# Optimization experiments

Measured on AMD Instinct MI355X. Metric: run time of the kernel, lower is better.

## Reference

```python
import jax, jax.numpy as jnp
import numpy as np

HQ, HKV, DK, DV = 8, 4, 128, 128
WIDTH, CLIP, MAXPOS = 16, 5.0, 2048
EPS = 1e-5

def rms_bn(x, g, ch_axis):
    # EMA_RMSBatchNorm (eval with batch stats): per-channel RMS over all other dims
    axes = tuple(i for i in range(x.ndim) if i != ch_axis)
    ms = jnp.mean(jnp.square(x), axis=axes, keepdims=True)
    shape = [1] * x.ndim; shape[ch_axis] = g.shape[0]
    return x * jax.lax.rsqrt(ms + EPS) * g.reshape(shape)

def ln(x, g, b):
    m = jnp.mean(x, -1, keepdims=True)
    v = jnp.mean(jnp.square(x - m), -1, keepdims=True)
    return (x - m) * jax.lax.rsqrt(v + EPS) * g + b

def rope(x):
    # x: [B,S,H,C], custom AlphaGenome frequency schedule
    B, S, H, C = x.shape
    nf = C // 2
    pos = jnp.arange(S, dtype=x.dtype)
    lin = jnp.arange(nf, dtype=x.dtype)
    end = max(MAXPOS - nf + 1.0, 1.0)
    geom = jnp.exp(jnp.linspace(0.0, np.log(end), nf).astype(x.dtype))
    inv_freq = 1.0 / (lin + geom)
    theta = jnp.repeat(pos[:, None] * inv_freq, 2, axis=-1)[None, :, None, :]  # [1,S,1,C]
    x_rot = jnp.stack([-x[..., 1::2], x[..., ::2]], axis=-1).reshape(x.shape)
    return x * jnp.cos(theta) + x_rot * jnp.sin(theta)

def _forward(x, pair_x, ab_bn_g, ab_fc_w, bn1_g, wq, wk, wv, qn_g, qn_b, kn_g, kn_b,
             vn_g, vn_b, wo, bo, bn2_g, mbn1_g, w1, b1, w2, b2, mbn2_g):
    B, S, C = x.shape
    # --- AttentionBias from pair representation ---
    pb = rms_bn(pair_x, ab_bn_g, 3)
    pb = jax.nn.gelu(pb, approximate=False)
    pb = jnp.einsum('bijc,gc->bijg', pb, ab_fc_w)          # [B,Sp,Sp,group]
    pb = jnp.repeat(jnp.repeat(pb, WIDTH, axis=1), WIDTH, axis=2)  # upsample to [B,S,S,group]
    bias = jnp.repeat(jnp.transpose(pb, (0, 3, 1, 2)), HKV, axis=1)  # [B,HQ,S,S]
    # --- GQA attention ---
    xn = rms_bn(x, bn1_g, 2)
    q = ln((xn @ wq.T).reshape(B, S, HQ, DK), qn_g, qn_b)
    k = ln((xn @ wk.T).reshape(B, S, HKV, DK), kn_g, kn_b)
    v = ln((xn @ wv.T).reshape(B, S, HKV, DV), vn_g, vn_b)
    q = rope(q); k = rope(k)
    rep = HQ // HKV
    k = jnp.tile(k, (1, 1, rep, 1))  # torch .repeat: [k0..k3, k0..k3]
    v = jnp.tile(v, (1, 1, rep, 1))
    logits = jnp.einsum('bshd,bThd->bhsT', q, k) / np.float32(np.sqrt(DK)) + bias
    logits = jnp.tanh(logits / CLIP) * CLIP
    attn = jax.nn.softmax(logits, axis=-1)
    y = jnp.einsum('bhsT,bThd->bshd', attn, v)
    # faithful to original: permute then reshape (layout scramble preserved)
    y = jnp.transpose(y, (0, 2, 1, 3)).reshape(B, S, HQ * DV)
    x = x + rms_bn(y @ wo.T + bo, bn2_g, 2)
    # --- MLP block ---
    h = jax.nn.relu(rms_bn(x, mbn1_g, 2) @ w1.T + b1)
    x = x + rms_bn(h @ w2.T + b2, mbn2_g, 2)
    return x, pair_x

def setup_inputs() -> dict:
    key = jax.random.key(0)
    ks = jax.random.split(key, 10)
    B, S, C, SP, PC = 2, 2048, 768, 128, 128
    n = lambda k, sh: jax.random.normal(k, sh, jnp.float32) * 0.02
    d = {}
    d['x'] = jax.random.normal(ks[0], (B, S, C), jnp.float32)
    d['pair_x'] = jax.random.normal(ks[1], (B, SP, SP, PC), jnp.float32)
    d['ab_bn_g'] = jnp.ones((PC,), jnp.float32)
    d['ab_fc_w'] = n(ks[2], (HQ // HKV, PC))
    d['bn1_g'] = jnp.ones((C,), jnp.float32)
    d['wq'] = n(ks[3], (HQ * DK, C))
    d['wk'] = n(ks[4], (HKV * DK, C))
    d['wv'] = n(ks[5], (HKV * DV, C))
    d['qn_g'] = jnp.ones((DK,), jnp.float32); d['qn_b'] = jnp.zeros((DK,), jnp.float32)
    d['kn_g'] = jnp.ones((DK,), jnp.float32); d['kn_b'] = jnp.zeros((DK,), jnp.float32)
    d['vn_g'] = jnp.ones((DV,), jnp.float32); d['vn_b'] = jnp.zeros((DV,), jnp.float32)
    d['wo'] = n(ks[6], (C, HQ * DV)); d['bo'] = jnp.zeros((C,), jnp.float32)
    d['bn2_g'] = jnp.ones((C,), jnp.float32)
    d['mbn1_g'] = jnp.ones((C,), jnp.float32)
    d['w1'] = n(ks[7], (2 * C, C)); d['b1'] = jnp.zeros((2 * C,), jnp.float32)
    d['w2'] = n(ks[8], (C, 2 * C)); d['b2'] = jnp.zeros((C,), jnp.float32)
    d['mbn2_g'] = jnp.ones((C,), jnp.float32)
    return d

def reference(x, pair_x, ab_bn_g, ab_fc_w, bn1_g, wq, wk, wv, qn_g, qn_b, kn_g, kn_b,
              vn_g, vn_b, wo, bo, bn2_g, mbn1_g, w1, b1, w2, b2, mbn2_g):
    return _forward(x, pair_x, ab_bn_g, ab_fc_w, bn1_g, wq, wk, wv, qn_g, qn_b, kn_g,
                    kn_b, vn_g, vn_b, wo, bo, bn2_g, mbn1_g, w1, b1, w2, b2, mbn2_g)
```

## Files before the change

kernel.cpp:

```cpp
#include <hip/hip_runtime.h>
#include <math.h>

#define EPS 1e-5f

typedef __attribute__((ext_vector_type(8))) short short8;
typedef __attribute__((ext_vector_type(4))) float f32x4;

namespace {

constexpr int Bn = 2, Sn = 2048, Cn = 768;
constexpr float INV_BS = 1.0f / 4096.0f;
constexpr float INV_PAIR = 1.0f / 32768.0f;
constexpr float LOG2E = 1.4426950408889634f;

__device__ __forceinline__ ushort f2bf(float f) {
  uint u = __float_as_uint(f);
  u = (u + 0x7fffu + ((u >> 16) & 1u)) >> 16;
  return (ushort)u;
}
__device__ __forceinline__ float bf2f(ushort u) {
  return __uint_as_float(((uint)u) << 16);
}
__device__ __forceinline__ uint cvt_pk_bf16(float lo, float hi) {
  uint r;
  asm("v_cvt_pk_bf16_f32 %0, %1, %2" : "=v"(r) : "v"(lo), "v"(hi));
  return r;
}
__device__ __forceinline__ void gl16(const ushort* g, ushort* l) {
  __builtin_amdgcn_global_load_lds(
      (const __attribute__((address_space(1))) unsigned int*)(unsigned long long)(size_t)g,
      (__attribute__((address_space(3))) unsigned int*)(unsigned int)(size_t)l, 16, 0, 0);
}

#define KSW(r, c) ((((r) * 128) + (c)) ^ (((r) & 7) * 8))
#define VTW(d, t) ((((d) * 64) + (t)) ^ (((d) & 7) * 8))
#define PSW2(w, q, c) ((w) * 2048 + ((((q) * 64) + (c)) ^ (((q) & 7) * 8)))

__global__ void castall_k(const float* __restrict__ wq, const float* __restrict__ wk,
                          const float* __restrict__ wv, const float* __restrict__ wo,
                          const float* __restrict__ w1, const float* __restrict__ w2,
                          ushort* __restrict__ dst) {
  int u = blockIdx.x * 256 + threadIdx.x;
  const float* src; int local;
  if (u < 98304)       { src = wq; local = u; }
  else if (u < 147456) { src = wk; local = u - 98304; }
  else if (u < 196608) { src = wv; local = u - 147456; }
  else if (u < 294912) { src = wo; local = u - 196608; }
  else if (u < 442368) { src = w1; local = u - 294912; }
  else                 { src = w2; local = u - 442368; }
  int i = local * 8;
  float4 a = *(const float4*)&src[i];
  float4 b = *(const float4*)&src[i + 4];
  union { short8 s8; ushort us[8]; } o;
  o.us[0] = f2bf(a.x); o.us[1] = f2bf(a.y); o.us[2] = f2bf(a.z); o.us[3] = f2bf(a.w);
  o.us[4] = f2bf(b.x); o.us[5] = f2bf(b.y); o.us[6] = f2bf(b.z); o.us[7] = f2bf(b.w);
  *(short8*)&dst[u * 8] = o.s8;
}

__global__ void rope_tab_k(float2* __restrict__ tab) {
  int idx = blockIdx.x * 256 + threadIdx.x;
  int s = idx >> 6, i = idx & 63;
  const float kGeo = logf(1985.0f) * (1.0f / 63.0f);
  float inv = 1.0f / ((float)i + expf((float)i * kGeo));
  float th = (float)s * inv;
  tab[idx] = make_float2(cosf(th), sinf(th));
}

__global__ void scale_cast_k(const float* __restrict__ a, const float* __restrict__ sums,
                             const float* __restrict__ g, ushort* __restrict__ o) {
  int idx = blockIdx.x * 256 + threadIdx.x;
  int c0 = (idx % 96) * 8;
  int base = idx * 8;
  float4 v0 = *(const float4*)&a[base];
  float4 v1 = *(const float4*)&a[base + 4];
  union { short8 s8; ushort us[8]; } r;
  float vv[8] = {v0.x, v0.y, v0.z, v0.w, v1.x, v1.y, v1.z, v1.w};
#pragma unroll
  for (int j = 0; j < 8; ++j) {
    float sc = rsqrtf(sums[c0 + j] * INV_BS + EPS) * g[c0 + j];
    r.us[j] = f2bf(vv[j] * sc);
  }
  *(short8*)&o[base] = r.s8;
}

__global__ void pair_sumsq_k(const float* __restrict__ p, float* __restrict__ out) {
  int r0 = blockIdx.x * 128;
  float acc = 0.f;
  for (int r = 0; r < 128; ++r) {
    float v = p[(size_t)(r0 + r) * 128 + threadIdx.x];
    acc += v * v;
  }
  atomicAdd(&out[threadIdx.x], acc);
}

__global__ void ch_sumsq768_k(const float* __restrict__ a, float* __restrict__ out) {
  int r0 = blockIdx.x * 16;
  int c = threadIdx.x;
  float acc = 0.f;
  for (int r = 0; r < 16; ++r) {
    float v = a[(size_t)(r0 + r) * 768 + c];
    acc += v * v;
  }
  atomicAdd(&out[c], acc);
}

__global__ void pair_bias_k(const float* __restrict__ p, const float* __restrict__ ps,
                            const float* __restrict__ g, const float* __restrict__ w,
                            float* __restrict__ pb2) {
  int idx = blockIdx.x * 128 + threadIdx.x;
  const float* row = p + (size_t)idx * 128;
  float a0 = 0.f, a1 = 0.f;
  for (int c = 0; c < 128; ++c) {
    float sc = rsqrtf(ps[c] * INV_PAIR + EPS) * g[c];
    float v = row[c] * sc;
    float ge = 0.5f * v * (1.f + erff(v * 0.70710678118654752f));
    a0 += ge * w[c];
    a1 += ge * w[128 + c];
  }
  pb2[(size_t)idx * 2 + 0] = a0 * (0.4f * LOG2E);
  pb2[(size_t)idx * 2 + 1] = a1 * (0.4f * LOG2E);
}

template <bool RELU, bool OUT_BF16>
__global__ __launch_bounds__(256) void gemm_bf16_k(
    const ushort* __restrict__ A, const ushort* __restrict__ B,
    void* __restrict__ Cv, int M, int N, int K,
    const float* __restrict__ bias) {
  __shared__ __align__(16) ushort As[128 * 64];
  __shared__ __align__(16) ushort Bs[128 * 64];
  const int m0 = blockIdx.y * 128, n0 = blockIdx.x * 128;
  const int tid = threadIdx.x;
  const int lane = tid & 63;
  const int wid = tid >> 6;
  const int l15 = lane & 15, l4 = lane >> 4;
  const int wm = (wid >> 1) * 64, wn = (wid & 1) * 64;
  const ushort* asrc[4]; const ushort* bsrc[4];
  ushort* adst[4]; ushort* bdst[4];
#pragma unroll
  for (int u = 0; u < 4; ++u) {
    int ci = u * 256 + tid;
    int r = ci >> 3, s = ci & 7, g = s ^ (r & 7);
    asrc[u] = A + (size_t)(m0 + r) * K + g * 8;
    bsrc[u] = B + (size_t)(n0 + r) * K + g * 8;
    adst[u] = &As[(u * 256 + wid * 64) * 8];
    bdst[u] = &Bs[(u * 256 + wid * 64) * 8];
  }
  f32x4 acc[4][4];
#pragma unroll
  for (int i = 0; i < 4; ++i)
#pragma unroll
    for (int j = 0; j < 4; ++j) acc[i][j] = (f32x4){0.f, 0.f, 0.f, 0.f};
  for (int k0 = 0; k0 < K; k0 += 64) {
#pragma unroll
    for (int u = 0; u < 4; ++u) {
      gl16(asrc[u] + k0, adst[u]);
      gl16(bsrc[u] + k0, bdst[u]);
    }
    __syncthreads();
#pragma unroll
    for (int ks = 0; ks < 2; ++ks) {
      const int sw = ((ks * 4 + l4) ^ (l15 & 7)) * 8;
      short8 af[4], bf[4];
#pragma unroll
      for (int i = 0; i < 4; ++i) af[i] = *(const short8*)&As[(wm + i * 16 + l15) * 64 + sw];
#pragma unroll
      for (int j = 0; j < 4; ++j) bf[j] = *(const short8*)&Bs[(wn + j * 16 + l15) * 64 + sw];
#pragma unroll
      for (int i = 0; i < 4; ++i)
#pragma unroll
        for (int j = 0; j < 4; ++j)
          acc[i][j] = __builtin_amdgcn_mfma_f32_16x16x32_bf16(af[i], bf[j], acc[i][j], 0, 0, 0);
    }
    __syncthreads();
  }
  float* Cf = (float*)Cv;
  ushort* Cb = (ushort*)Cv;
#pragma unroll
  for (int j = 0; j < 4; ++j) {
    int col = n0 + wn + j * 16 + l15;
    float bv = bias ? bias[col] : 0.f;
#pragma unroll
    for (int i = 0; i < 4; ++i) {
      int row = m0 + wm + i * 16 + l4 * 4;
#pragma unroll
      for (int r = 0; r < 4; ++r) {
        float v = acc[i][j][r] + bv;
        if (RELU) v = fmaxf(v, 0.f);
        if (OUT_BF16) Cb[(size_t)(row + r) * N + col] = f2bf(v);
        else Cf[(size_t)(row + r) * N + col] = v;
      }
    }
  }
}

template <bool SUMSQ>
__global__ __launch_bounds__(256) void gemm64_bf16_k(
    const ushort* __restrict__ A, const ushort* __restrict__ B,
    float* __restrict__ Cf, int M, int N, int K,
    const float* __restrict__ bias, float* __restrict__ ssq) {
  __shared__ __align__(16) ushort As[64 * 64];
  __shared__ __align__(16) ushort Bs[128 * 64];
  const int m0 = blockIdx.y * 64, n0 = blockIdx.x * 128;
  const int tid = threadIdx.x;
  const int lane = tid & 63;
  const int wid = tid >> 6;
  const int l15 = lane & 15, l4 = lane >> 4;
  const int wn = wid * 32;
  const ushort* asrc[2]; ushort* adst[2];
  const ushort* bsrc[4]; ushort* bdst[4];
#pragma unroll
  for (int u = 0; u < 2; ++u) {
    int ci = u * 256 + tid;
    int r = ci >> 3, s = ci & 7, g = s ^ (r & 7);
    asrc[u] = A + (size_t)(m0 + r) * K + g * 8;
    adst[u] = &As[(u * 256 + wid * 64) * 8];
  }
#pragma unroll
  for (int u = 0; u < 4; ++u) {
    int ci = u * 256 + tid;
    int r = ci >> 3, s = ci & 7, g = s ^ (r & 7);
    bsrc[u] = B + (size_t)(n0 + r) * K + g * 8;
    bdst[u] = &Bs[(u * 256 + wid * 64) * 8];
  }
  f32x4 acc[4][2];
#pragma unroll
  for (int i = 0; i < 4; ++i)
#pragma unroll
    for (int j = 0; j < 2; ++j) acc[i][j] = (f32x4){0.f, 0.f, 0.f, 0.f};
  for (int k0 = 0; k0 < K; k0 += 64) {
#pragma unroll
    for (int u = 0; u < 2; ++u) gl16(asrc[u] + k0, adst[u]);
#pragma unroll
    for (int u = 0; u < 4; ++u) gl16(bsrc[u] + k0, bdst[u]);
    __syncthreads();
#pragma unroll
    for (int ks = 0; ks < 2; ++ks) {
      const int sw = ((ks * 4 + l4) ^ (l15 & 7)) * 8;
      short8 af[4], bf[2];
#pragma unroll
      for (int i = 0; i < 4; ++i) af[i] = *(const short8*)&As[(i * 16 + l15) * 64 + sw];
#pragma unroll
      for (int j = 0; j < 2; ++j) bf[j] = *(const short8*)&Bs[(wn + j * 16 + l15) * 64 + sw];
#pragma unroll
      for (int i = 0; i < 4; ++i)
#pragma unroll
        for (int j = 0; j < 2; ++j)
          acc[i][j] = __builtin_amdgcn_mfma_f32_16x16x32_bf16(af[i], bf[j], acc[i][j], 0, 0, 0);
    }
    __syncthreads();
  }
#pragma unroll
  for (int j = 0; j < 2; ++j) {
    int col = n0 + wn + j * 16 + l15;
    float bv = bias ? bias[col] : 0.f;
    float sq = 0.f;
#pragma unroll
    for (int i = 0; i < 4; ++i) {
      int row = m0 + i * 16 + l4 * 4;
#pragma unroll
      for (int r = 0; r < 4; ++r) {
        float v = acc[i][j][r] + bv;
        if (SUMSQ) sq += v * v;
        Cf[(size_t)(row + r) * N + col] = v;
      }
    }
    if (SUMSQ) {
      sq += __shfl_xor(sq, 16);
      sq += __shfl_xor(sq, 32);
      if (l4 == 0) atomicAdd(&ssq[col], sq);
    }
  }
}

__global__ __launch_bounds__(256) void ln_rope_k(
    const float* __restrict__ qkv, const float2* __restrict__ rtab,
    const float* __restrict__ qg, const float* __restrict__ qb,
    const float* __restrict__ kg, const float* __restrict__ kb,
    const float* __restrict__ vg, const float* __restrict__ vb,
    ushort* __restrict__ q_b, ushort* __restrict__ k_b, ushort* __restrict__ v_b) {
  const int half = threadIdx.x >> 7;
  const int tid = threadIdx.x & 127;
  const int bs = blockIdx.x * 2 + half;
  const int slot = blockIdx.y;
  const int s = bs & (Sn - 1);
  const int b = bs >> 11;
  const float* src; const float* g; const float* be; ushort* dst; bool dorope; bool isq = false;
  if (slot < 8) {
    src = qkv + (size_t)bs * 2048 + slot * 128;
    g = qg; be = qb;
    dst = q_b + ((size_t)(b * 8 + slot) * Sn + s) * 128;
    dorope = true; isq = true;
  } else if (slot < 12) {
    int h = slot - 8;
    src = qkv + (size_t)bs * 2048 + 1024 + h * 128;
    g = kg; be = kb;
    dst = k_b + ((size_t)(b * 4 + h) * Sn + s) * 128;
    dorope = true;
  } else {
    int h = slot - 12;
    src = qkv + (size_t)bs * 2048 + 1536 + h * 128;
    g = vg; be = vb;
    dst = v_b + ((size_t)(b * 4 + h) * Sn + s) * 128;
    dorope = false;
  }
  __shared__ float sh[2][128];
  __shared__ float red[2][4];
  float v = src[tid];
  float sum = v;
#pragma unroll
  for (int o = 32; o >= 1; o >>= 1) sum += __shfl_xor(sum, o);
  if ((tid & 63) == 0) red[half][tid >> 6] = sum;
  __syncthreads();
  float mean = (red[half][0] + red[half][1]) * (1.f / 128.f);
  float d = v - mean;
  float s2 = d * d;
#pragma unroll
  for (int o = 32; o >= 1; o >>= 1) s2 += __shfl_xor(s2, o);
  if ((tid & 63) == 0) red[half][2 + (tid >> 6)] = s2;
  __syncthreads();
  float var = (red[half][2] + red[half][3]) * (1.f / 128.f);
  float val = d * rsqrtf(var + EPS) * g[tid] + be[tid];
  if (dorope) {
    sh[half][tid] = val;
    __syncthreads();
    float2 cssn = rtab[(s << 6) | (tid >> 1)];
    float rot = (tid & 1) ? sh[half][tid - 1] : -sh[half][tid + 1];
    val = val * cssn.x + rot * cssn.y;
  }
  if (isq) val *= 0.035355339059327376f * LOG2E;
  dst[tid] = f2bf(val);
}

__global__ __launch_bounds__(256) void vtrans_k(const ushort* __restrict__ vb,
                                                ushort* __restrict__ vtt) {
  __shared__ __align__(16) ushort T[64][136];
  const int hv = blockIdx.y, s0 = blockIdx.x * 64;
  const int tid = threadIdx.x;
  const ushort* src = vb + ((size_t)hv * Sn + s0) * 128;
#pragma unroll
  for (int u = 0; u < 4; ++u) {
    int fi = u * 256 + tid;
    int r = fi >> 4, c = (fi & 15) * 8;
    *(float4*)&T[r][c] = *(const float4*)&src[(size_t)r * 128 + c];
  }
  __syncthreads();
  ushort* dst = vtt + (size_t)hv * 128 * Sn + s0;
#pragma unroll
  for (int u = 0; u < 4; ++u) {
    int fi = u * 256 + tid;
    int d = fi >> 3, t8 = (fi & 7) * 8;
    union { float4 f4; ushort us[8]; } o;
#pragma unroll
    for (int j = 0; j < 8; ++j) o.us[j] = T[t8 + j][d];
    *(float4*)&dst[(size_t)d * Sn + t8] = o.f4;
  }
}

__global__ __launch_bounds__(256, 2) void flash_v10_k(
    const ushort* __restrict__ qb, const ushort* __restrict__ kb,
    const ushort* __restrict__ vtt, const float* __restrict__ pb2,
    ushort* __restrict__ part_y, float* __restrict__ part_l) {
  __shared__ __align__(16) ushort Ks[64 * 128];
  __shared__ __align__(16) ushort Vt[128 * 64];
  __shared__ __align__(16) ushort Ps[4 * 32 * 64];
  const int s0 = blockIdx.x * 128;
  const int bh = blockIdx.y;
  const int half = blockIdx.z;
  const int b = bh >> 3, h = bh & 7;
  const int kv = h & 3, grp = h >> 2;
  const int tid = threadIdx.x;
  const int wid = tid >> 6, lane = tid & 63;
  const int l15 = lane & 15, l4 = lane >> 4;
  const ushort* kbase = kb + (size_t)(b * 4 + kv) * Sn * 128;
  const ushort* vbase = vtt + (size_t)(b * 4 + kv) * 128 * Sn;
  const int qr0 = s0 + wid * 32;
  short8 qf[2][4];
#pragma unroll
  for (int rg = 0; rg < 2; ++rg)
#pragma unroll
    for (int kc = 0; kc < 4; ++kc)
      qf[rg][kc] = *(const short8*)&qb[((size_t)bh * Sn + qr0 + rg * 16 + l15) * 128 + kc * 32 + l4 * 8];
  const ushort* ksrc[4]; const ushort* vsrc[4];
  ushort* kdst[4]; ushort* vdst[4];
#pragma unroll
  for (int u = 0; u < 4; ++u) {
    int ci = u * 256 + tid;
    int kr = ci >> 4, kg = (ci & 15) ^ (kr & 7);
    ksrc[u] = kbase + (size_t)kr * 128 + kg * 8;
    kdst[u] = &Ks[(u * 256 + wid * 64) * 8];
    int vd = ci >> 3, vg = (ci & 7) ^ (vd & 7);
    vsrc[u] = vbase + (size_t)vd * Sn + vg * 8;
    vdst[u] = &Vt[(u * 256 + wid * 64) * 8];
  }
  f32x4 y[2][8];
#pragma unroll
  for (int rg = 0; rg < 2; ++rg)
#pragma unroll
    for (int i = 0; i < 8; ++i) y[rg][i] = (f32x4){0.f, 0.f, 0.f, 0.f};
  float lsum[2] = {0.f, 0.f};
  const float C2 = -10.f * LOG2E;
  const int tbeg = half * 704;
  const int tend = (half == 2) ? 2048 : tbeg + 704;
  for (int t0 = tbeg; t0 < tend; t0 += 64) {
    __syncthreads();
#pragma unroll
    for (int u = 0; u < 4; ++u) {
      gl16(ksrc[u] + (size_t)t0 * 128, kdst[u]);
      gl16(vsrc[u] + t0, vdst[u]);
    }
    __syncthreads();
    f32x4 acc[2][4];
#pragma unroll
    for (int rg = 0; rg < 2; ++rg)
#pragma unroll
      for (int nb = 0; nb < 4; ++nb) acc[rg][nb] = (f32x4){0.f, 0.f, 0.f, 0.f};
    __builtin_amdgcn_s_setprio(1);
#pragma unroll
    for (int kc = 0; kc < 4; ++kc)
#pragma unroll
      for (int nb = 0; nb < 4; ++nb) {
        short8 kf = *(const short8*)&Ks[KSW(nb * 16 + l15, kc * 32 + l4 * 8)];
        acc[0][nb] = __builtin_amdgcn_mfma_f32_16x16x32_bf16(kf, qf[0][kc], acc[0][nb], 0, 0, 0);
        acc[1][nb] = __builtin_amdgcn_mfma_f32_16x16x32_bf16(kf, qf[1][kc], acc[1][nb], 0, 0, 0);
      }
    __builtin_amdgcn_s_setprio(0);
#pragma unroll
    for (int rg = 0; rg < 2; ++rg)
#pragma unroll
      for (int nb = 0; nb < 4; ++nb) {
        float bias = pb2[(((size_t)b * 128 + (s0 >> 4) + wid * 2 + rg) * 128 + (t0 >> 4) + nb) * 2 + grp];
        float p[4];
#pragma unroll
        for (int r = 0; r < 4; ++r) {
          float e = exp2f(acc[rg][nb][r] + bias);
          p[r] = exp2f(C2 * __builtin_amdgcn_rcpf(e + 1.f));
        }
        lsum[rg] += (p[0] + p[1]) + (p[2] + p[3]);
        uint2 pk;
        pk.x = cvt_pk_bf16(p[0], p[1]);
        pk.y = cvt_pk_bf16(p[2], p[3]);
        *(uint2*)&Ps[PSW2(wid, rg * 16 + l15, nb * 16 + l4 * 4)] = pk;
      }
    __builtin_amdgcn_s_setprio(1);
#pragma unroll
    for (int ks = 0; ks < 2; ++ks) {
      short8 pa0 = *(const short8*)&Ps[PSW2(wid, l15, ks * 32 + l4 * 8)];
      short8 pa1 = *(const short8*)&Ps[PSW2(wid, 16 + l15, ks * 32 + l4 * 8)];
#pragma unroll
      for (int nbd = 0; nbd < 8; ++nbd) {
        short8 vf = *(const short8*)&Vt[VTW(nbd * 16 + l15, ks * 32 + l4 * 8)];
        y[0][nbd] = __builtin_amdgcn_mfma_f32_16x16x32_bf16(pa0, vf, y[0][nbd], 0, 0, 0);
        y[1][nbd] = __builtin_amdgcn_mfma_f32_16x16x32_bf16(pa1, vf, y[1][nbd], 0, 0, 0);
      }
    }
    __builtin_amdgcn_s_setprio(0);
  }
#pragma unroll
  for (int rg = 0; rg < 2; ++rg) {
    float ls = lsum[rg];
    ls += __shfl_xor(ls, 16);
    ls += __shfl_xor(ls, 32);
    if (l4 == 0) part_l[(size_t)(half * 16 + bh) * Sn + qr0 + rg * 16 + l15] = ls;
    ushort* pybase = part_y + ((size_t)(half * 16 + bh) * Sn + qr0 + rg * 16) * 128;
#pragma unroll
    for (int nbd = 0; nbd < 8; ++nbd)
#pragma unroll
      for (int r = 0; r < 4; ++r)
        pybase[(size_t)(l4 * 4 + r) * 128 + nbd * 16 + l15] = f2bf(y[rg][nbd][r]);
  }
}

__global__ void combine_k(const ushort* __restrict__ part_y, const float* __restrict__ part_l,
                          ushort* __restrict__ attn_b) {
  int t = blockIdx.x * 256 + threadIdx.x;
  int row = t >> 4;
  size_t o0 = (size_t)row * 128 + (t & 15) * 8;
  float acc[8] = {};
#pragma unroll
  for (int hf = 0; hf < 3; ++hf) {
    union { short8 s8; ushort us[8]; } u;
    u.s8 = *(const short8*)&part_y[o0 + (size_t)hf * 4194304];
#pragma unroll
    for (int j = 0; j < 8; ++j) acc[j] += bf2f(u.us[j]);
  }
  float rcp = 1.f / (part_l[row] + part_l[row + 32768] + part_l[row + 65536]);
  union { short8 s8; ushort us[8]; } o;
#pragma unroll
  for (int j = 0; j < 8; ++j) o.us[j] = f2bf(acc[j] * rcp);
  *(short8*)&attn_b[o0] = o.s8;
}

template <bool SUMSQ>
__global__ void add_scale_k(const float* __restrict__ base, const float* __restrict__ delta,
                            const float* __restrict__ sums, const float* __restrict__ g,
                            float* __restrict__ out, float* __restrict__ ssq) {
  const int c = threadIdx.x;
  const float sc = rsqrtf(sums[c] * INV_BS + EPS) * g[c];
  const int r0 = blockIdx.x * 16;
  float sq = 0.f;
  for (int r = 0; r < 16; ++r) {
    size_t idx = (size_t)(r0 + r) * 768 + c;
    float v = base[idx] + delta[idx] * sc;
    out[idx] = v;
    if (SUMSQ) sq += v * v;
  }
  if (SUMSQ) atomicAdd(&ssq[c], sq);
}

}

extern "C" void kernel_launch(void* const* d_in, const int* in_sizes, int n_in,
                              void* d_out, int out_size, void* d_ws, size_t ws_size,
                              hipStream_t stream) {
  const float* x       = (const float*)d_in[0];
  const float* pair_x  = (const float*)d_in[1];
  const float* ab_bn_g = (const float*)d_in[2];
  const float* ab_fc_w = (const float*)d_in[3];
  const float* bn1_g   = (const float*)d_in[4];
  const float* wq      = (const float*)d_in[5];
  const float* wk      = (const float*)d_in[6];
  const float* wv      = (const float*)d_in[7];
  const float* qn_g    = (const float*)d_in[8];
  const float* qn_b    = (const float*)d_in[9];
  const float* kn_g    = (const float*)d_in[10];
  const float* kn_b    = (const float*)d_in[11];
  const float* vn_g    = (const float*)d_in[12];
  const float* vn_b    = (const float*)d_in[13];
  const float* wo      = (const float*)d_in[14];
  const float* bo      = (const float*)d_in[15];
  const float* bn2_g   = (const float*)d_in[16];
  const float* mbn1_g  = (const float*)d_in[17];
  const float* w1      = (const float*)d_in[18];
  const float* b1      = (const float*)d_in[19];
  const float* w2      = (const float*)d_in[20];
  const float* b2      = (const float*)d_in[21];
  const float* mbn2_g  = (const float*)d_in[22];
  float* out = (float*)d_out;
  float* ws = (float*)d_ws;

  float* ps    = ws + 0;
  float* xs    = ws + 256;
  float* es    = ws + 1024;
  float* x2s   = ws + 2048;
  float* fs    = ws + 3072;
  float* pb2   = ws + 4096;
  ushort* wall_b = (ushort*)(ws + 69632);
  ushort* wo_b = (ushort*)(ws + 856064);
  ushort* w1_b = (ushort*)(ws + 1249280);
  ushort* w2_b = (ushort*)(ws + 1839104);
  ushort* xn_b = (ushort*)(ws + 2428928);
  float* qkvtmp = ws + 4001792;
  ushort* q_b  = (ushort*)(ws + 12390400);
  ushort* k_b  = (ushort*)(ws + 14487552);
  ushort* v_b  = (ushort*)(ws + 15536128);
  float2* rtab = (float2*)(ws + 16584704);
  ushort* v_tt = (ushort*)(ws + 2428928);
  ushort* part_y = (ushort*)(ws + 3477504);
  float* part_l = ws + 11866112;
  ushort* attn_b = (ushort*)(ws + 11997184);
  float* proj  = ws + 3477504;
  float* x2    = ws + 6623232;
  ushort* x2n_b = (ushort*)(ws + 9768960);
  ushort* hbuf_b = (ushort*)(ws + 3477504);
  float* proj2 = ws + 11341824;

  (void)hipMemsetAsync(ws, 0, 4096 * sizeof(float), stream);

  castall_k<<<2304, 256, 0, stream>>>(wq, wk, wv, wo, w1, w2, wall_b);
  rope_tab_k<<<512, 256, 0, stream>>>(rtab);

  pair_sumsq_k<<<256, 128, 0, stream>>>(pair_x, ps);
  pair_bias_k<<<256, 128, 0, stream>>>(pair_x, ps, ab_bn_g, ab_fc_w, pb2);
  ch_sumsq768_k<<<256, 768, 0, stream>>>(x, xs);
  scale_cast_k<<<1536, 256, 0, stream>>>(x, xs, bn1_g, xn_b);
  gemm_bf16_k<false, false><<<dim3(16, 32), 256, 0, stream>>>(xn_b, wall_b, qkvtmp, 4096, 2048, 768, nullptr);
  ln_rope_k<<<dim3(2048, 16), 256, 0, stream>>>(qkvtmp, rtab, qn_g, qn_b, kn_g, kn_b,
                                                vn_g, vn_b, q_b, k_b, v_b);
  vtrans_k<<<dim3(32, 8), 256, 0, stream>>>(v_b, v_tt);
  flash_v10_k<<<dim3(16, 16, 3), 256, 0, stream>>>(q_b, k_b, v_tt, pb2, part_y, part_l);
  combine_k<<<2048, 256, 0, stream>>>(part_y, part_l, attn_b);
  gemm64_bf16_k<true><<<dim3(6, 64), 256, 0, stream>>>(attn_b, wo_b, proj, 4096, 768, 1024, bo, es);
  add_scale_k<true><<<256, 768, 0, stream>>>(x, proj, es, bn2_g, x2, x2s);
  scale_cast_k<<<1536, 256, 0, stream>>>(x2, x2s, mbn1_g, x2n_b);
  gemm_bf16_k<true, true><<<dim3(12, 32), 256, 0, stream>>>(x2n_b, w1_b, hbuf_b, 4096, 1536, 768, b1);
  gemm64_bf16_k<true><<<dim3(6, 64), 256, 0, stream>>>(hbuf_b, w2_b, proj2, 4096, 768, 1536, b2, fs);
  add_scale_k<false><<<256, 768, 0, stream>>>(x2, proj2, fs, mbn2_g, out, nullptr);

  (void)hipMemcpyAsync(out + 3145728, pair_x, (size_t)4194304 * sizeof(float),
                       hipMemcpyDeviceToDevice, stream);
}
```

Baseline: 295.0 us.

## Double-buffer K/V tiles in flash attention and split KV into four chunks

Flash attention now preloads the first K/V tile and, each iteration, issues the next tile's global-to-LDS loads into a second buffer before computing on the current one, removing one barrier per iteration. The KV dimension is split into four equal 512-token chunks instead of three uneven ones, increasing grid parallelism, and the combine kernel now sums four partials. This doubles K/V LDS usage and requires the partial-output workspace to hold a fourth slice.

```diff
diff --git a/kernel.cpp b/kernel.cpp
--- a/kernel.cpp
+++ b/kernel.cpp
@@ -356,12 +356,12 @@
   }
 }
 
-__global__ __launch_bounds__(256, 2) void flash_v10_k(
+__global__ __launch_bounds__(256, 2) void flash_v12_k(
     const ushort* __restrict__ qb, const ushort* __restrict__ kb,
     const ushort* __restrict__ vtt, const float* __restrict__ pb2,
     ushort* __restrict__ part_y, float* __restrict__ part_l) {
-  __shared__ __align__(16) ushort Ks[64 * 128];
-  __shared__ __align__(16) ushort Vt[128 * 64];
+  __shared__ __align__(16) ushort Ks[2 * 64 * 128];
+  __shared__ __align__(16) ushort Vt[2 * 128 * 64];
   __shared__ __align__(16) ushort Ps[4 * 32 * 64];
   const int s0 = blockIdx.x * 128;
   const int bh = blockIdx.y;
@@ -381,16 +381,13 @@
     for (int kc = 0; kc < 4; ++kc)
       qf[rg][kc] = *(const short8*)&qb[((size_t)bh * Sn + qr0 + rg * 16 + l15) * 128 + kc * 32 + l4 * 8];
   const ushort* ksrc[4]; const ushort* vsrc[4];
-  ushort* kdst[4]; ushort* vdst[4];
 #pragma unroll
   for (int u = 0; u < 4; ++u) {
     int ci = u * 256 + tid;
     int kr = ci >> 4, kg = (ci & 15) ^ (kr & 7);
     ksrc[u] = kbase + (size_t)kr * 128 + kg * 8;
-    kdst[u] = &Ks[(u * 256 + wid * 64) * 8];
     int vd = ci >> 3, vg = (ci & 7) ^ (vd & 7);
     vsrc[u] = vbase + (size_t)vd * Sn + vg * 8;
-    vdst[u] = &Vt[(u * 256 + wid * 64) * 8];
   }
   f32x4 y[2][8];
 #pragma unroll
@@ -399,16 +396,25 @@
     for (int i = 0; i < 8; ++i) y[rg][i] = (f32x4){0.f, 0.f, 0.f, 0.f};
   float lsum[2] = {0.f, 0.f};
   const float C2 = -10.f * LOG2E;
-  const int tbeg = half * 704;
-  const int tend = (half == 2) ? 2048 : tbeg + 704;
-  for (int t0 = tbeg; t0 < tend; t0 += 64) {
-    __syncthreads();
-#pragma unroll
-    for (int u = 0; u < 4; ++u) {
-      gl16(ksrc[u] + (size_t)t0 * 128, kdst[u]);
-      gl16(vsrc[u] + t0, vdst[u]);
-    }
-    __syncthreads();
+  const int tbeg = half * 512;
+#pragma unroll
+  for (int u = 0; u < 4; ++u) {
+    gl16(ksrc[u] + (size_t)tbeg * 128, &Ks[(u * 256 + wid * 64) * 8]);
+    gl16(vsrc[u] + tbeg, &Vt[(u * 256 + wid * 64) * 8]);
+  }
+  __syncthreads();
+  int cur = 0;
+  for (int it = 0; it < 8; ++it) {
+    const int t0 = tbeg + it * 64;
+    if (it < 7) {
+      const int nb_off = (cur ^ 1) * 8192;
+#pragma unroll
+      for (int u = 0; u < 4; ++u) {
+        gl16(ksrc[u] + (size_t)(t0 + 64) * 128, &Ks[nb_off + (u * 256 + wid * 64) * 8]);
+        gl16(vsrc[u] + t0 + 64, &Vt[nb_off + (u * 256 + wid * 64) * 8]);
+      }
+    }
+    const int cb = cur * 8192;
     f32x4 acc[2][4];
 #pragma unroll
     for (int rg = 0; rg < 2; ++rg)
@@ -419,7 +425,7 @@
     for (int kc = 0; kc < 4; ++kc)
 #pragma unroll
       for (int nb = 0; nb < 4; ++nb) {
-        short8 kf = *(const short8*)&Ks[KSW(nb * 16 + l15, kc * 32 + l4 * 8)];
+        short8 kf = *(const short8*)&Ks[cb + KSW(nb * 16 + l15, kc * 32 + l4 * 8)];
         acc[0][nb] = __builtin_amdgcn_mfma_f32_16x16x32_bf16(kf, qf[0][kc], acc[0][nb], 0, 0, 0);
         acc[1][nb] = __builtin_amdgcn_mfma_f32_16x16x32_bf16(kf, qf[1][kc], acc[1][nb], 0, 0, 0);
       }
@@ -448,12 +454,14 @@
       short8 pa1 = *(const short8*)&Ps[PSW2(wid, 16 + l15, ks * 32 + l4 * 8)];
 #pragma unroll
       for (int nbd = 0; nbd < 8; ++nbd) {
-        short8 vf = *(const short8*)&Vt[VTW(nbd * 16 + l15, ks * 32 + l4 * 8)];
+        short8 vf = *(const short8*)&Vt[cb + VTW(nbd * 16 + l15, ks * 32 + l4 * 8)];
         y[0][nbd] = __builtin_amdgcn_mfma_f32_16x16x32_bf16(pa0, vf, y[0][nbd], 0, 0, 0);
         y[1][nbd] = __builtin_amdgcn_mfma_f32_16x16x32_bf16(pa1, vf, y[1][nbd], 0, 0, 0);
       }
     }
     __builtin_amdgcn_s_setprio(0);
+    __syncthreads();
+    cur ^= 1;
   }
 #pragma unroll
   for (int rg = 0; rg < 2; ++rg) {
@@ -477,13 +485,13 @@
   size_t o0 = (size_t)row * 128 + (t & 15) * 8;
   float acc[8] = {};
 #pragma unroll
-  for (int hf = 0; hf < 3; ++hf) {
+  for (int hf = 0; hf < 4; ++hf) {
     union { short8 s8; ushort us[8]; } u;
     u.s8 = *(const short8*)&part_y[o0 + (size_t)hf * 4194304];
 #pragma unroll
     for (int j = 0; j < 8; ++j) acc[j] += bf2f(u.us[j]);
   }
-  float rcp = 1.f / (part_l[row] + part_l[row + 32768] + part_l[row + 65536]);
+  float rcp = 1.f / (part_l[row] + part_l[row + 32768] + part_l[row + 65536] + part_l[row + 98304]);
   union { short8 s8; ushort us[8]; } o;
 #pragma unroll
   for (int j = 0; j < 8; ++j) o.us[j] = f2bf(acc[j] * rcp);
@@ -577,7 +585,7 @@
   ln_rope_k<<<dim3(2048, 16), 256, 0, stream>>>(qkvtmp, rtab, qn_g, qn_b, kn_g, kn_b,
                                                 vn_g, vn_b, q_b, k_b, v_b);
   vtrans_k<<<dim3(32, 8), 256, 0, stream>>>(v_b, v_tt);
-  flash_v10_k<<<dim3(16, 16, 3), 256, 0, stream>>>(q_b, k_b, v_tt, pb2, part_y, part_l);
+  flash_v12_k<<<dim3(16, 16, 4), 256, 0, stream>>>(q_b, k_b, v_tt, pb2, part_y, part_l);
   combine_k<<<2048, 256, 0, stream>>>(part_y, part_l, attn_b);
   gemm64_bf16_k<true><<<dim3(6, 64), 256, 0, stream>>>(attn_b, wo_b, proj, 4096, 768, 1024, bo, es);
   add_scale_k<true><<<256, 768, 0, stream>>>(x, proj, es, bn2_g, x2, x2s);
```

New measurement: 291.0 us. About the same (-1.3%).
